# Optimization experiments

Hardware: AMD Instinct MI355X
Metric: run time of the kernel (lower is better)

## Reference

```python
import jax, jax.numpy as jnp
import numpy as np

B, N, I, O, R = 8, 1024, 256, 256, 8


def setup_inputs() -> dict:
    key = jax.random.key(0)
    k1, k2, k3 = jax.random.split(key, 3)
    x = jax.random.normal(k1, (B, N, I), dtype=jnp.float32)
    adj = jax.random.uniform(k2, (B, N, N, R), dtype=jnp.float32)  # soft adjacency [b, src, dst, r]
    weight = jax.random.normal(k3, (R, I, O), dtype=jnp.float32)   # per-relation transform
    return {"x": x, "adj": adj, "weight": weight}


def reference(x, adj, weight):
    # per-relation transformed features: [b, src, r, o]
    f = jnp.einsum('bni,rio->bnro', x, weight)
    # contraction over source nodes and relations, weighted by soft adjacency:
    # out[b, dst, o] = sum_{src, r} adj[b, src, dst, r] * f[b, src, r, o]
    out = jnp.einsum('bnro,bnmr->bmo', f, adj)
    # normalization: total incoming soft-edge weight per destination node
    denom = jnp.clip(adj.sum(axis=(1, 3)), 1e-16, None)  # [b, dst]
    return out / denom[..., None]
```

## Files before the change

### kernel.cpp

```cpp
#include <hip/hip_runtime.h>
#include <stdint.h>


typedef float          floatx4  __attribute__((ext_vector_type(4)));
typedef short          shortx8  __attribute__((ext_vector_type(8)));
typedef unsigned short ushortx4 __attribute__((ext_vector_type(4)));
typedef unsigned short ushortx8 __attribute__((ext_vector_type(8)));

__device__ __forceinline__ unsigned short f2bf(float f) {
  union { float f; unsigned int u; } v; v.f = f;
  unsigned int u = v.u + 0x7FFFu + ((v.u >> 16) & 1u);
  return (unsigned short)(u >> 16);
}

__device__ __forceinline__ void gload16(const void* g, void* l) {
  __builtin_amdgcn_global_load_lds((__attribute__((address_space(1))) void*)g,
                                   (__attribute__((address_space(3))) void*)l,
                                   16, 0, 0);
}

#define FENCE_KEEP4 asm volatile("s_waitcnt vmcnt(4) lgkmcnt(0)" ::: "memory")
#define FENCE_ALL   asm volatile("s_waitcnt vmcnt(0) lgkmcnt(0)" ::: "memory")
#define MEMFENCE    asm volatile("" ::: "memory")

__global__ __launch_bounds__(256) void prep_xw(const float* __restrict__ x,
                                               const float* __restrict__ w,
                                               unsigned short* __restrict__ xbf,
                                               unsigned short* __restrict__ wt) {
  int bid = blockIdx.x;
  if (bid < 1024) {
    int t = bid * 256 + threadIdx.x;
    const float4* p = (const float4*)x + (size_t)t * 2;
    float4 a = p[0], b4 = p[1];
    ushortx8 o;
    o[0] = f2bf(a.x);  o[1] = f2bf(a.y);  o[2] = f2bf(a.z);  o[3] = f2bf(a.w);
    o[4] = f2bf(b4.x); o[5] = f2bf(b4.y); o[6] = f2bf(b4.z); o[7] = f2bf(b4.w);
    *(ushortx8*)(xbf + (size_t)t * 8) = o;
  } else {
    int id = (bid - 1024) * 256 + threadIdx.x;
    int r = id >> 16, i = (id >> 8) & 255, o = id & 255;
    float v = w[((size_t)(r * 256 + i) << 8) + o];
    wt[((size_t)(o * 8 + r) << 8) + i] = f2bf(v);
  }
}

__global__ __launch_bounds__(256) void k1_gemm(const unsigned short* __restrict__ xbf,
                                               const unsigned short* __restrict__ wt,
                                               unsigned short* __restrict__ ft) {
  int bid = blockIdx.x;
  int p0 = (bid & 15) * 128, q0 = (bid >> 4) * 128;
  int l = threadIdx.x & 63, w = threadIdx.x >> 6;
  int lr = l & 15, lg = l >> 4;
  int pw = p0 + (w >> 1) * 64, qw = q0 + (w & 1) * 64;

  floatx4 acc[4][4] = {};
#pragma unroll
  for (int ks = 0; ks < 8; ++ks) {
    shortx8 a[4], b[4];
#pragma unroll
    for (int pi = 0; pi < 4; ++pi)
      a[pi] = *(const shortx8*)(wt + (size_t)(pw + pi * 16 + lr) * 256 + ks * 32 + lg * 8);
#pragma unroll
    for (int qi = 0; qi < 4; ++qi)
      b[qi] = *(const shortx8*)(xbf + (size_t)(qw + qi * 16 + lr) * 256 + ks * 32 + lg * 8);
#pragma unroll
    for (int pi = 0; pi < 4; ++pi)
#pragma unroll
      for (int qi = 0; qi < 4; ++qi)
        acc[pi][qi] = __builtin_amdgcn_mfma_f32_16x16x32_bf16(a[pi], b[qi], acc[pi][qi], 0, 0, 0);
  }
#pragma unroll
  for (int pi = 0; pi < 4; ++pi) {
    int nbase = pw + pi * 16 + lg * 4;
    int o = nbase >> 3, rb = nbase & 7;
#pragma unroll
    for (int qi = 0; qi < 4; ++qi) {
      int m = qw + qi * 16 + lr;
      int b8 = m >> 10, src = m & 1023;
      ushortx4 h;
      h[0] = f2bf(acc[pi][qi][0]); h[1] = f2bf(acc[pi][qi][1]);
      h[2] = f2bf(acc[pi][qi][2]); h[3] = f2bf(acc[pi][qi][3]);
      *(ushortx4*)(ft + ((size_t)(b8 * 256 + o) << 13) + src * 8 + rb) = h;
    }
  }
}

#define ASZ (64 * 64)
#define BSZ (128 * 64)
__global__ __launch_bounds__(512, 4) void k2_gemm(const float* __restrict__ adj,
                                                  const unsigned short* __restrict__ ft,
                                                  float* __restrict__ pout,
                                                  float* __restrict__ dpart) {
  __shared__ __align__(16) unsigned short Alds[3 * ASZ];
  __shared__ __align__(16) unsigned short Blds[3 * BSZ];

  int bid = blockIdx.x;
  int b = bid & 7;
  int o0 = ((bid >> 3) & 1) * 128;
  int kc = (bid >> 4) & 1;
  int dst0 = (bid >> 5) * 64;

  int t = threadIdx.x, l = t & 63, w = t >> 6;
  int lr = l & 15, lg = l >> 4;
  int wm = w >> 2, wo = w & 3;

  int dst_l = (t >> 1) & 63;
  int rh = (t & 1) * 4;
  int sA = t >> 7;
  int csw = (l & 7) ^ (l >> 3);

  const size_t adj_b = (size_t)b << 23;
  const unsigned short* ftb = ft + ((size_t)b << 21);
  const int src_base = kc * 512;

  float dsum = 0.f;
  floatx4 acc[2][2] = {};
  float4 av0[2], av1[2];

  auto A_load = [&](int kt, float4* v) {
#pragma unroll
    for (int j = 0; j < 2; ++j) {
      int src = src_base + kt * 8 + sA + j * 4;
      v[j] = *(const float4*)(adj + adj_b + ((size_t)src << 13)
                              + ((size_t)(dst0 + dst_l) << 3) + rh);
    }
  };
  auto A_store = [&](int buf, const float4* v) {
#pragma unroll
    for (int j = 0; j < 2; ++j) {
      int src_l = sA + j * 4;
      float4 q = v[j];
      dsum += q.x + q.y + q.z + q.w;
      ushortx4 h;
      h[0] = f2bf(q.x); h[1] = f2bf(q.y); h[2] = f2bf(q.z); h[3] = f2bf(q.w);
      int slot = src_l ^ (dst_l & 7);
      *(ushortx4*)&Alds[buf * ASZ + dst_l * 64 + slot * 8 + rh] = h;
    }
  };
  auto B_stage = [&](int kt, int buf) {
    int kbase = (src_base + kt * 8) * 8;
#pragma unroll
    for (int i = 0; i < 2; ++i) {
      int orow = w * 16 + i * 8 + (l >> 3);
      const unsigned short* g = ftb + ((size_t)(o0 + orow) << 13) + kbase + (csw << 3);
      gload16(g, &Blds[buf * BSZ + (w * 16 + i * 8) * 64]);
    }
  };
  auto compute = [&](int buf) {
#pragma unroll
    for (int s = 0; s < 2; ++s) {
      int slotbase = s * 4 + lg;
      shortx8 af[2], bfr[2];
#pragma unroll
      for (int mi = 0; mi < 2; ++mi) {
        int arow = wm * 32 + mi * 16 + lr;
        af[mi] = *(const shortx8*)&Alds[buf * ASZ + arow * 64 + ((slotbase ^ (arow & 7)) << 3)];
      }
#pragma unroll
      for (int ni = 0; ni < 2; ++ni) {
        int brow = wo * 32 + ni * 16 + lr;
        bfr[ni] = *(const shortx8*)&Blds[buf * BSZ + brow * 64 + ((slotbase ^ (brow & 7)) << 3)];
      }
#pragma unroll
      for (int mi = 0; mi < 2; ++mi)
#pragma unroll
        for (int ni = 0; ni < 2; ++ni)
          acc[mi][ni] = __builtin_amdgcn_mfma_f32_16x16x32_bf16(af[mi], bfr[ni], acc[mi][ni], 0, 0, 0);
    }
  };

#define STEP(kt, C0, C1, C2, RIN, ROUT, ISS, ST)                       \
  {                                                                    \
    if (ISS) { A_load((kt) + 2, ROUT); B_stage((kt) + 2, C2); }        \
    if (ST)  A_store(C1, RIN);                                         \
    compute(C0);                                                       \
    if (ST) {                                                          \
      if (ISS) { FENCE_KEEP4; } else { FENCE_ALL; }                    \
      __builtin_amdgcn_s_barrier();                                    \
      MEMFENCE;                                                        \
    }                                                                  \
  }

  B_stage(0, 0);
  A_load(0, av0);
  A_load(1, av1);
  B_stage(1, 1);
  A_store(0, av0);
  FENCE_KEEP4;
  __builtin_amdgcn_s_barrier();
  MEMFENCE;

  for (int kt0 = 0; kt0 < 60; kt0 += 6) {
    STEP(kt0 + 0, 0, 1, 2, av1, av0, 1, 1);
    STEP(kt0 + 1, 1, 2, 0, av0, av1, 1, 1);
    STEP(kt0 + 2, 2, 0, 1, av1, av0, 1, 1);
    STEP(kt0 + 3, 0, 1, 2, av0, av1, 1, 1);
    STEP(kt0 + 4, 1, 2, 0, av1, av0, 1, 1);
    STEP(kt0 + 5, 2, 0, 1, av0, av1, 1, 1);
  }
  STEP(60, 0, 1, 2, av1, av0, 1, 1);
  STEP(61, 1, 2, 0, av0, av1, 1, 1);
  STEP(62, 2, 0, 1, av1, av0, 0, 1);
  STEP(63, 0, 1, 2, av0, av1, 0, 0);
#undef STEP
  __syncthreads();

  float* dsf = (float*)Alds;
  dsf[t] = dsum;
  __syncthreads();
  if (t < 64) {
    float s = 0.f;
#pragma unroll
    for (int sl = 0; sl < 4; ++sl) {
      s += dsf[sl * 128 + t * 2];
      s += dsf[sl * 128 + t * 2 + 1];
    }
    dpart[kc * 8192 + (b << 10) + dst0 + t] = s;
  }

#pragma unroll
  for (int mi = 0; mi < 2; ++mi) {
#pragma unroll
    for (int reg = 0; reg < 4; ++reg) {
      int row = dst0 + wm * 32 + mi * 16 + lg * 4 + reg;
#pragma unroll
      for (int ni = 0; ni < 2; ++ni) {
        int col = o0 + wo * 32 + ni * 16 + lr;
        pout[(size_t)kc * 2097152 + (((size_t)b << 10) + row) * 256 + col] = acc[mi][ni][reg];
      }
    }
  }
}

__global__ __launch_bounds__(256) void k3_reduce(const float* __restrict__ pout,
                                                 const float* __restrict__ dpart,
                                                 float* __restrict__ outp) {
  int bid = blockIdx.x;
  size_t base = (size_t)bid * 256 + threadIdx.x;
  float v = pout[base] + pout[2097152 + base];
  float d = dpart[bid] + dpart[8192 + bid];
  outp[base] = v / fmaxf(d, 1e-16f);
}

extern "C" void kernel_launch(void* const* d_in, const int* in_sizes, int n_in,
                              void* d_out, int out_size, void* d_ws, size_t ws_size,
                              hipStream_t stream) {
  const float* x   = (const float*)d_in[0];
  const float* adj = (const float*)d_in[1];
  const float* w   = (const float*)d_in[2];
  float* out = (float*)d_out;

  char* ws = (char*)d_ws;
  unsigned short* ft  = (unsigned short*)(ws);
  unsigned short* xbf = (unsigned short*)(ws + 33554432);
  unsigned short* wt  = (unsigned short*)(ws + 37748736);
  float* pout  = (float*)(ws + 38797312);
  float* dpart = (float*)(ws + 55574528);

  prep_xw<<<3072, 256, 0, stream>>>(x, w, xbf, wt);
  k1_gemm<<<1024, 256, 0, stream>>>(xbf, wt, ft);
  k2_gemm<<<512, 512, 0, stream>>>(adj, ft, pout, dpart);
  k3_reduce<<<8192, 256, 0, stream>>>(pout, dpart, out);
}
```

Before: 137.0 us.

## Register-stage B tile and deepen prefetch to four A and three B tiles

Replaces the direct global-to-LDS loads of the B tile with ordinary global loads into registers, followed by swizzled LDS stores. The software pipeline is restructured around register prefetch queues four tiles deep for A and three for B, and LDS drops from triple to double buffering. Explicit vmcnt waits are removed so the compiler tracks outstanding loads. The bf16 packing now uses the HIP intrinsic two values at a time. The aim is more memory-latency hiding with less LDS, at the cost of more registers and extra LDS store instructions, which may reduce occupancy.

Result: slower. 202.4 us (+47.7%).

```diff
diff --git a/kernel.cpp b/kernel.cpp
--- a/kernel.cpp
+++ b/kernel.cpp
@@ -1,4 +1,5 @@
 #include <hip/hip_runtime.h>
+#include <hip/hip_bf16.h>
 #include <stdint.h>
 
 
@@ -6,6 +7,8 @@
 typedef short          shortx8  __attribute__((ext_vector_type(8)));
 typedef unsigned short ushortx4 __attribute__((ext_vector_type(4)));
 typedef unsigned short ushortx8 __attribute__((ext_vector_type(8)));
+typedef unsigned int   uintx2   __attribute__((ext_vector_type(2)));
+typedef unsigned int   uintx4   __attribute__((ext_vector_type(4)));
 
 __device__ __forceinline__ unsigned short f2bf(float f) {
   union { float f; unsigned int u; } v; v.f = f;
@@ -13,15 +16,14 @@
   return (unsigned short)(u >> 16);
 }
 
-__device__ __forceinline__ void gload16(const void* g, void* l) {
-  __builtin_amdgcn_global_load_lds((__attribute__((address_space(1))) void*)g,
-                                   (__attribute__((address_space(3))) void*)l,
-                                   16, 0, 0);
-}
-
-#define FENCE_KEEP4 asm volatile("s_waitcnt vmcnt(4) lgkmcnt(0)" ::: "memory")
-#define FENCE_ALL   asm volatile("s_waitcnt vmcnt(0) lgkmcnt(0)" ::: "memory")
-#define MEMFENCE    asm volatile("" ::: "memory")
+__device__ __forceinline__ unsigned int pkbf(float a, float b) {
+  __hip_bfloat16 ha = __float2bfloat16(a), hb = __float2bfloat16(b);
+  unsigned short ua, ub;
+  __builtin_memcpy(&ua, &ha, 2); __builtin_memcpy(&ub, &hb, 2);
+  return (unsigned int)ua | ((unsigned int)ub << 16);
+}
+
+#define MEMFENCE asm volatile("" ::: "memory")
 
 __global__ __launch_bounds__(256) void prep_xw(const float* __restrict__ x,
                                                const float* __restrict__ w,
@@ -91,8 +93,8 @@
                                                   const unsigned short* __restrict__ ft,
                                                   float* __restrict__ pout,
                                                   float* __restrict__ dpart) {
-  __shared__ __align__(16) unsigned short Alds[3 * ASZ];
-  __shared__ __align__(16) unsigned short Blds[3 * BSZ];
+  __shared__ __align__(16) unsigned short Alds[2 * ASZ];
+  __shared__ __align__(16) unsigned short Blds[2 * BSZ];
 
   int bid = blockIdx.x;
   int b = bid & 7;
@@ -107,15 +109,15 @@
   int dst_l = (t >> 1) & 63;
   int rh = (t & 1) * 4;
   int sA = t >> 7;
-  int csw = (l & 7) ^ (l >> 3);
 
   const size_t adj_b = (size_t)b << 23;
   const unsigned short* ftb = ft + ((size_t)b << 21);
   const int src_base = kc * 512;
 
-  float dsum = 0.f;
+  float d0 = 0.f, d1 = 0.f;
   floatx4 acc[2][2] = {};
-  float4 av0[2], av1[2];
+  float4 av0[2], av1[2], av2[2], av3[2];
+  uintx4 bv0[2], bv1[2], bv2[2];
 
   auto A_load = [&](int kt, float4* v) {
 #pragma unroll
@@ -130,20 +132,26 @@
     for (int j = 0; j < 2; ++j) {
       int src_l = sA + j * 4;
       float4 q = v[j];
-      dsum += q.x + q.y + q.z + q.w;
-      ushortx4 h;
-      h[0] = f2bf(q.x); h[1] = f2bf(q.y); h[2] = f2bf(q.z); h[3] = f2bf(q.w);
+      d0 += q.x + q.z; d1 += q.y + q.w;
+      uintx2 h; h[0] = pkbf(q.x, q.y); h[1] = pkbf(q.z, q.w);
       int slot = src_l ^ (dst_l & 7);
-      *(ushortx4*)&Alds[buf * ASZ + dst_l * 64 + slot * 8 + rh] = h;
-    }
-  };
-  auto B_stage = [&](int kt, int buf) {
+      *(uintx2*)&Alds[buf * ASZ + dst_l * 64 + slot * 8 + rh] = h;
+    }
+  };
+  auto B_load = [&](int kt, uintx4* v) {
     int kbase = (src_base + kt * 8) * 8;
 #pragma unroll
     for (int i = 0; i < 2; ++i) {
-      int orow = w * 16 + i * 8 + (l >> 3);
-      const unsigned short* g = ftb + ((size_t)(o0 + orow) << 13) + kbase + (csw << 3);
-      gload16(g, &Blds[buf * BSZ + (w * 16 + i * 8) * 64]);
+      int orow = o0 + w * 16 + i * 8 + (l >> 3);
+      v[i] = *(const uintx4*)(ftb + ((size_t)orow << 13) + kbase + ((l & 7) << 3));
+    }
+  };
+  auto B_store = [&](int buf, const uintx4* v) {
+#pragma unroll
+    for (int i = 0; i < 2; ++i) {
+      int row = w * 16 + i * 8 + (l >> 3);
+      int swc = (l & 7) ^ (l >> 3);
+      *(uintx4*)&Blds[buf * BSZ + row * 64 + swc * 8] = v[i];
     }
   };
   auto compute = [&](int buf) {
@@ -169,44 +177,49 @@
     }
   };
 
-#define STEP(kt, C0, C1, C2, RIN, ROUT, ISS, ST)                       \
+#define STEP(kt, AVL, AVS, BVL, BVS, CUR, NXT, ISSA, ISSB, ST)         \
   {                                                                    \
-    if (ISS) { A_load((kt) + 2, ROUT); B_stage((kt) + 2, C2); }        \
-    if (ST)  A_store(C1, RIN);                                         \
-    compute(C0);                                                       \
+    if (ISSA) A_load((kt) + 4, AVL);                                   \
+    if (ISSB) B_load((kt) + 3, BVL);                                   \
+    if (ST) { A_store(NXT, AVS); B_store(NXT, BVS); }                  \
+    compute(CUR);                                                      \
     if (ST) {                                                          \
-      if (ISS) { FENCE_KEEP4; } else { FENCE_ALL; }                    \
+      asm volatile("s_waitcnt lgkmcnt(0)" ::: "memory");               \
       __builtin_amdgcn_s_barrier();                                    \
       MEMFENCE;                                                        \
     }                                                                  \
   }
 
-  B_stage(0, 0);
-  A_load(0, av0);
-  A_load(1, av1);
-  B_stage(1, 1);
-  A_store(0, av0);
-  FENCE_KEEP4;
+  A_load(0, av0); A_load(1, av1); A_load(2, av2); A_load(3, av3);
+  B_load(0, bv0); B_load(1, bv1); B_load(2, bv2);
+  A_store(0, av0); B_store(0, bv0);
+  asm volatile("s_waitcnt lgkmcnt(0)" ::: "memory");
   __builtin_amdgcn_s_barrier();
   MEMFENCE;
 
-  for (int kt0 = 0; kt0 < 60; kt0 += 6) {
-    STEP(kt0 + 0, 0, 1, 2, av1, av0, 1, 1);
-    STEP(kt0 + 1, 1, 2, 0, av0, av1, 1, 1);
-    STEP(kt0 + 2, 2, 0, 1, av1, av0, 1, 1);
-    STEP(kt0 + 3, 0, 1, 2, av0, av1, 1, 1);
-    STEP(kt0 + 4, 1, 2, 0, av1, av0, 1, 1);
-    STEP(kt0 + 5, 2, 0, 1, av0, av1, 1, 1);
-  }
-  STEP(60, 0, 1, 2, av1, av0, 1, 1);
-  STEP(61, 1, 2, 0, av0, av1, 1, 1);
-  STEP(62, 2, 0, 1, av1, av0, 0, 1);
-  STEP(63, 0, 1, 2, av0, av1, 0, 0);
+  for (int kt0 = 0; kt0 < 60; kt0 += 12) {
+    STEP(kt0 + 0,  av0, av1, bv0, bv1, 0, 1, 1, 1, 1);
+    STEP(kt0 + 1,  av1, av2, bv1, bv2, 1, 0, 1, 1, 1);
+    STEP(kt0 + 2,  av2, av3, bv2, bv0, 0, 1, 1, 1, 1);
+    STEP(kt0 + 3,  av3, av0, bv0, bv1, 1, 0, 1, 1, 1);
+    STEP(kt0 + 4,  av0, av1, bv1, bv2, 0, 1, 1, 1, 1);
+    STEP(kt0 + 5,  av1, av2, bv2, bv0, 1, 0, 1, 1, 1);
+    STEP(kt0 + 6,  av2, av3, bv0, bv1, 0, 1, 1, 1, 1);
+    STEP(kt0 + 7,  av3, av0, bv1, bv2, 1, 0, 1, 1, 1);
+    STEP(kt0 + 8,  av0, av1, bv2, bv0, 0, 1, 1, 1, 1);
+    STEP(kt0 + 9,  av1, av2, bv0, bv1, 1, 0, 1, 1, 1);
+    STEP(kt0 + 10, av2, av3, bv1, bv2, 0, 1, 1, 1, 1);
+    STEP(kt0 + 11, av3, av0, bv2, bv0, 1, 0, 1, 1, 1);
+  }
+  STEP(60, av0, av1, bv0, bv1, 0, 1, 0, 1, 1);
+  STEP(61, av1, av2, bv1, bv2, 1, 0, 0, 0, 1);
+  STEP(62, av2, av3, bv2, bv0, 0, 1, 0, 0, 1);
+  STEP(63, av3, av0, bv0, bv1, 1, 0, 0, 0, 0);
 #undef STEP
   __syncthreads();
 
   float* dsf = (float*)Alds;
-  dsf[t] = dsum;
+  dsf[t] = d0 + d1;
   __syncthreads();
   if (t < 64) {
     float s = 0.f;
```

## Load adjacency directly into MFMA A-fragment registers, bypassing LDS staging

Applied to the files above, without the earlier changes.

Each wave now loads its own adjacency values from global memory straight into the register layout the MFMA A operand expects and converts them to bf16 in registers. This removes the A tile's LDS buffers, the LDS store and read traffic, and the final LDS reduction for the denominator, which is now done with wave shuffles. In exchange, the four waves sharing a row block each reload the same adjacency data instead of sharing it through LDS, raising global and cache traffic, and register pressure grows from holding two stages of float4 prefetches.

New measurement: 173.4 us. 1.27x slower.

```diff
diff --git a/kernel.cpp b/kernel.cpp
--- a/kernel.cpp
+++ b/kernel.cpp
@@ -1,4 +1,5 @@
 #include <hip/hip_runtime.h>
+#include <hip/hip_bf16.h>
 #include <stdint.h>
 
 
@@ -13,15 +14,22 @@
   return (unsigned short)(u >> 16);
 }
 
+__device__ __forceinline__ unsigned int pkbf(float a, float b) {
+  return ((unsigned int)f2bf(a)) | (((unsigned int)f2bf(b)) << 16);
+}
+
+__device__ __forceinline__ shortx8 cvt8(float4 a, float4 b) {
+  union { unsigned int u[4]; shortx8 s; } r;
+  r.u[0] = pkbf(a.x, a.y); r.u[1] = pkbf(a.z, a.w);
+  r.u[2] = pkbf(b.x, b.y); r.u[3] = pkbf(b.z, b.w);
+  return r.s;
+}
+
 __device__ __forceinline__ void gload16(const void* g, void* l) {
   __builtin_amdgcn_global_load_lds((__attribute__((address_space(1))) void*)g,
                                    (__attribute__((address_space(3))) void*)l,
                                    16, 0, 0);
 }
-
-#define FENCE_KEEP4 asm volatile("s_waitcnt vmcnt(4) lgkmcnt(0)" ::: "memory")
-#define FENCE_ALL   asm volatile("s_waitcnt vmcnt(0) lgkmcnt(0)" ::: "memory")
-#define MEMFENCE    asm volatile("" ::: "memory")
 
 __global__ __launch_bounds__(256) void prep_xw(const float* __restrict__ x,
                                                const float* __restrict__ w,
@@ -85,13 +93,11 @@
   }
 }
 
-#define ASZ (64 * 64)
 #define BSZ (128 * 64)
 __global__ __launch_bounds__(512, 4) void k2_gemm(const float* __restrict__ adj,
                                                   const unsigned short* __restrict__ ft,
                                                   float* __restrict__ pout,
                                                   float* __restrict__ dpart) {
-  __shared__ __align__(16) unsigned short Alds[3 * ASZ];
   __shared__ __align__(16) unsigned short Blds[3 * BSZ];
 
   int bid = blockIdx.x;
@@ -103,42 +109,30 @@
   int t = threadIdx.x, l = t & 63, w = t >> 6;
   int lr = l & 15, lg = l >> 4;
   int wm = w >> 2, wo = w & 3;
-
-  int dst_l = (t >> 1) & 63;
-  int rh = (t & 1) * 4;
-  int sA = t >> 7;
-  int csw = (l & 7) ^ (l >> 3);
-
-  const size_t adj_b = (size_t)b << 23;
+  bool wq0 = (wo == 0);
+
+  const int src_base = kc * 512;
+  const float* adjp = adj + ((size_t)b << 23) + ((size_t)src_base << 13)
+                    + ((size_t)(dst0 + wm * 32 + lr) << 3) + ((size_t)lg << 13);
   const unsigned short* ftb = ft + ((size_t)b << 21);
-  const int src_base = kc * 512;
-
-  float dsum = 0.f;
+
+  float dd[2] = {0.f, 0.f};
   floatx4 acc[2][2] = {};
-  float4 av0[2], av1[2];
-
-  auto A_load = [&](int kt, float4* v) {
-#pragma unroll
-    for (int j = 0; j < 2; ++j) {
-      int src = src_base + kt * 8 + sA + j * 4;
-      v[j] = *(const float4*)(adj + adj_b + ((size_t)src << 13)
-                              + ((size_t)(dst0 + dst_l) << 3) + rh);
-    }
-  };
-  auto A_store = [&](int buf, const float4* v) {
-#pragma unroll
-    for (int j = 0; j < 2; ++j) {
-      int src_l = sA + j * 4;
-      float4 q = v[j];
-      dsum += q.x + q.y + q.z + q.w;
-      ushortx4 h;
-      h[0] = f2bf(q.x); h[1] = f2bf(q.y); h[2] = f2bf(q.z); h[3] = f2bf(q.w);
-      int slot = src_l ^ (dst_l & 7);
-      *(ushortx4*)&Alds[buf * ASZ + dst_l * 64 + slot * 8 + rh] = h;
-    }
+  float4 aE[2][2][2], aO[2][2][2];
+
+  auto A_load = [&](int kt, float4 (&v)[2][2][2]) {
+#pragma unroll
+    for (int mi = 0; mi < 2; ++mi)
+#pragma unroll
+      for (int s = 0; s < 2; ++s)
+#pragma unroll
+        for (int j = 0; j < 2; ++j)
+          v[mi][s][j] = *(const float4*)(adjp + (size_t)kt * 65536
+                                         + s * 32768 + mi * 128 + j * 4);
   };
   auto B_stage = [&](int kt, int buf) {
     int kbase = (src_base + kt * 8) * 8;
+    int csw = (l & 7) ^ (l >> 3);
 #pragma unroll
     for (int i = 0; i < 2; ++i) {
       int orow = w * 16 + i * 8 + (l >> 3);
@@ -146,76 +140,71 @@
       gload16(g, &Blds[buf * BSZ + (w * 16 + i * 8) * 64]);
     }
   };
-  auto compute = [&](int buf) {
-#pragma unroll
-    for (int s = 0; s < 2; ++s) {
-      int slotbase = s * 4 + lg;
-      shortx8 af[2], bfr[2];
-#pragma unroll
-      for (int mi = 0; mi < 2; ++mi) {
-        int arow = wm * 32 + mi * 16 + lr;
-        af[mi] = *(const shortx8*)&Alds[buf * ASZ + arow * 64 + ((slotbase ^ (arow & 7)) << 3)];
-      }
-#pragma unroll
-      for (int ni = 0; ni < 2; ++ni) {
-        int brow = wo * 32 + ni * 16 + lr;
-        bfr[ni] = *(const shortx8*)&Blds[buf * BSZ + brow * 64 + ((slotbase ^ (brow & 7)) << 3)];
-      }
-#pragma unroll
-      for (int mi = 0; mi < 2; ++mi)
-#pragma unroll
-        for (int ni = 0; ni < 2; ++ni)
-          acc[mi][ni] = __builtin_amdgcn_mfma_f32_16x16x32_bf16(af[mi], bfr[ni], acc[mi][ni], 0, 0, 0);
-    }
-  };
-
-#define STEP(kt, C0, C1, C2, RIN, ROUT, ISS, ST)                       \
-  {                                                                    \
-    if (ISS) { A_load((kt) + 2, ROUT); B_stage((kt) + 2, C2); }        \
-    if (ST)  A_store(C1, RIN);                                         \
-    compute(C0);                                                       \
-    if (ST) {                                                          \
-      if (ISS) { FENCE_KEEP4; } else { FENCE_ALL; }                    \
-      __builtin_amdgcn_s_barrier();                                    \
-      MEMFENCE;                                                        \
-    }                                                                  \
+
+#define STEP(kt, C0, C1, C2, AC, ISS, ST)                                        \
+  {                                                                              \
+    if (ISS) B_stage((kt) + 2, C2);                                              \
+    __builtin_amdgcn_sched_barrier(0);                                           \
+    shortx8 af[2][2];                                                            \
+    _Pragma("unroll") for (int s = 0; s < 2; ++s)                                \
+      _Pragma("unroll") for (int mi = 0; mi < 2; ++mi) {                         \
+        float4 p = AC[mi][s][0], q = AC[mi][s][1];                               \
+        af[s][mi] = cvt8(p, q);                                                  \
+        if (wq0) dd[mi] += ((p.x + p.y) + (p.z + p.w)) + ((q.x + q.y) + (q.z + q.w)); \
+      }                                                                          \
+    if (ISS) A_load((kt) + 2, AC);                                               \
+    _Pragma("unroll") for (int s = 0; s < 2; ++s) {                              \
+      int slotbase = s * 4 + lg;                                                 \
+      shortx8 bfr[2];                                                            \
+      _Pragma("unroll") for (int ni = 0; ni < 2; ++ni) {                         \
+        int brow = wo * 32 + ni * 16 + lr;                                       \
+        bfr[ni] = *(const shortx8*)&Blds[(C0) * BSZ + brow * 64 + ((slotbase ^ (brow & 7)) << 3)]; \
+      }                                                                          \
+      _Pragma("unroll") for (int mi = 0; mi < 2; ++mi)                           \
+        _Pragma("unroll") for (int ni = 0; ni < 2; ++ni)                         \
+          acc[mi][ni] = __builtin_amdgcn_mfma_f32_16x16x32_bf16(af[s][mi], bfr[ni], acc[mi][ni], 0, 0, 0); \
+    }                                                                            \
+    if (ST) {                                                                    \
+      if (ISS) { asm volatile("s_waitcnt vmcnt(10)" ::: "memory"); }             \
+      else     { asm volatile("s_waitcnt vmcnt(0)"  ::: "memory"); }             \
+      __builtin_amdgcn_s_barrier();                                              \
+      asm volatile("" ::: "memory");                                             \
+    }                                                                            \
   }
 
   B_stage(0, 0);
-  A_load(0, av0);
-  A_load(1, av1);
   B_stage(1, 1);
-  A_store(0, av0);
-  FENCE_KEEP4;
+  __builtin_amdgcn_sched_barrier(0);
+  A_load(0, aE);
+  A_load(1, aO);
+  asm volatile("s_waitcnt vmcnt(0)" ::: "memory");
   __builtin_amdgcn_s_barrier();
-  MEMFENCE;
+  asm volatile("" ::: "memory");
 
   for (int kt0 = 0; kt0 < 60; kt0 += 6) {
-    STEP(kt0 + 0, 0, 1, 2, av1, av0, 1, 1);
-    STEP(kt0 + 1, 1, 2, 0, av0, av1, 1, 1);
-    STEP(kt0 + 2, 2, 0, 1, av1, av0, 1, 1);
-    STEP(kt0 + 3, 0, 1, 2, av0, av1, 1, 1);
-    STEP(kt0 + 4, 1, 2, 0, av1, av0, 1, 1);
-    STEP(kt0 + 5, 2, 0, 1, av0, av1, 1, 1);
-  }
-  STEP(60, 0, 1, 2, av1, av0, 1, 1);
-  STEP(61, 1, 2, 0, av0, av1, 1, 1);
-  STEP(62, 2, 0, 1, av1, av0, 0, 1);
-  STEP(63, 0, 1, 2, av0, av1, 0, 0);
+    STEP(kt0 + 0, 0, 1, 2, aE, 1, 1);
+    STEP(kt0 + 1, 1, 2, 0, aO, 1, 1);
+    STEP(kt0 + 2, 2, 0, 1, aE, 1, 1);
+    STEP(kt0 + 3, 0, 1, 2, aO, 1, 1);
+    STEP(kt0 + 4, 1, 2, 0, aE, 1, 1);
+    STEP(kt0 + 5, 2, 0, 1, aO, 1, 1);
+  }
+  STEP(60, 0, 1, 2, aE, 1, 1);
+  STEP(61, 1, 2, 0, aO, 1, 1);
+  STEP(62, 2, 0, 1, aE, 0, 1);
+  STEP(63, 0, 1, 2, aO, 0, 0);
 #undef STEP
-  __syncthreads();
-
-  float* dsf = (float*)Alds;
-  dsf[t] = dsum;
-  __syncthreads();
-  if (t < 64) {
-    float s = 0.f;
-#pragma unroll
-    for (int sl = 0; sl < 4; ++sl) {
-      s += dsf[sl * 128 + t * 2];
-      s += dsf[sl * 128 + t * 2 + 1];
-    }
-    dpart[kc * 8192 + (b << 10) + dst0 + t] = s;
+
+  if (wq0) {
+#pragma unroll
+    for (int mi = 0; mi < 2; ++mi) {
+      dd[mi] += __shfl_xor(dd[mi], 16);
+      dd[mi] += __shfl_xor(dd[mi], 32);
+    }
+    if (l < 16) {
+      dpart[kc * 8192 + (b << 10) + dst0 + wm * 32 + lr]      = dd[0];
+      dpart[kc * 8192 + (b << 10) + dst0 + wm * 32 + 16 + lr] = dd[1];
+    }
   }
 
 #pragma unroll
```

## Deepen k2 pipeline to prefetch distance three with 4-stage B buffers

Applied to the files above, without the earlier changes.

Restructures the k2 GEMM main loop so the B tile (bf16 transformed features) is staged three iterations ahead in four LDS buffers. The A tile (fp32 adjacency) moves to a double-buffered LDS layout whose loads are held in registers three steps ahead. Waits become vmcnt(8) with sched_barriers around the s_barrier, so more global loads stay in flight across each barrier. The bf16 conversion now uses the HIP intrinsic. This aims to hide global memory latency, at the cost of more LDS and registers per block, which could reduce occupancy.

New measurement: 134.1 us, median of 2. -2.1%, faster.

```diff
diff --git a/kernel.cpp b/kernel.cpp
--- a/kernel.cpp
+++ b/kernel.cpp
@@ -1,4 +1,5 @@
 #include <hip/hip_runtime.h>
+#include <hip/hip_bf16.h>
 #include <stdint.h>
 
 
@@ -8,9 +9,9 @@
 typedef unsigned short ushortx8 __attribute__((ext_vector_type(8)));
 
 __device__ __forceinline__ unsigned short f2bf(float f) {
-  union { float f; unsigned int u; } v; v.f = f;
-  unsigned int u = v.u + 0x7FFFu + ((v.u >> 16) & 1u);
-  return (unsigned short)(u >> 16);
+  __hip_bfloat16 h = __float2bfloat16(f);
+  unsigned short u; __builtin_memcpy(&u, &h, 2);
+  return u;
 }
 
 __device__ __forceinline__ void gload16(const void* g, void* l) {
@@ -18,10 +19,6 @@
                                    (__attribute__((address_space(3))) void*)l,
                                    16, 0, 0);
 }
-
-#define FENCE_KEEP4 asm volatile("s_waitcnt vmcnt(4) lgkmcnt(0)" ::: "memory")
-#define FENCE_ALL   asm volatile("s_waitcnt vmcnt(0) lgkmcnt(0)" ::: "memory")
-#define MEMFENCE    asm volatile("" ::: "memory")
 
 __global__ __launch_bounds__(256) void prep_xw(const float* __restrict__ x,
                                                const float* __restrict__ w,
@@ -85,14 +82,14 @@
   }
 }
 
-#define ASZ (64 * 64)
+#define ASZ 4096
 #define BSZ (128 * 64)
 __global__ __launch_bounds__(512, 4) void k2_gemm(const float* __restrict__ adj,
                                                   const unsigned short* __restrict__ ft,
                                                   float* __restrict__ pout,
                                                   float* __restrict__ dpart) {
-  __shared__ __align__(16) unsigned short Alds[3 * ASZ];
-  __shared__ __align__(16) unsigned short Blds[3 * BSZ];
+  __shared__ __align__(16) unsigned short Alds[2 * ASZ];
+  __shared__ __align__(16) unsigned short Blds[4 * BSZ];
 
   int bid = blockIdx.x;
   int b = bid & 7;
@@ -115,7 +112,7 @@
 
   float dsum = 0.f;
   floatx4 acc[2][2] = {};
-  float4 av0[2], av1[2];
+  float4 avA[2], avB[2];
 
   auto A_load = [&](int kt, float4* v) {
 #pragma unroll
@@ -125,7 +122,7 @@
                               + ((size_t)(dst0 + dst_l) << 3) + rh);
     }
   };
-  auto A_store = [&](int buf, const float4* v) {
+  auto A_store = [&](int abuf, const float4* v) {
 #pragma unroll
     for (int j = 0; j < 2; ++j) {
       int src_l = sA + j * 4;
@@ -134,7 +131,7 @@
       ushortx4 h;
       h[0] = f2bf(q.x); h[1] = f2bf(q.y); h[2] = f2bf(q.z); h[3] = f2bf(q.w);
       int slot = src_l ^ (dst_l & 7);
-      *(ushortx4*)&Alds[buf * ASZ + dst_l * 64 + slot * 8 + rh] = h;
+      *(ushortx4*)&Alds[abuf * ASZ + dst_l * 64 + slot * 8 + rh] = h;
     }
   };
   auto B_stage = [&](int kt, int buf) {
@@ -146,7 +143,7 @@
       gload16(g, &Blds[buf * BSZ + (w * 16 + i * 8) * 64]);
     }
   };
-  auto compute = [&](int buf) {
+  auto compute = [&](int bbuf, int abuf) {
 #pragma unroll
     for (int s = 0; s < 2; ++s) {
       int slotbase = s * 4 + lg;
@@ -154,12 +151,12 @@
 #pragma unroll
       for (int mi = 0; mi < 2; ++mi) {
         int arow = wm * 32 + mi * 16 + lr;
-        af[mi] = *(const shortx8*)&Alds[buf * ASZ + arow * 64 + ((slotbase ^ (arow & 7)) << 3)];
+        af[mi] = *(const shortx8*)&Alds[abuf * ASZ + arow * 64 + ((slotbase ^ (arow & 7)) << 3)];
       }
 #pragma unroll
       for (int ni = 0; ni < 2; ++ni) {
         int brow = wo * 32 + ni * 16 + lr;
-        bfr[ni] = *(const shortx8*)&Blds[buf * BSZ + brow * 64 + ((slotbase ^ (brow & 7)) << 3)];
+        bfr[ni] = *(const shortx8*)&Blds[bbuf * BSZ + brow * 64 + ((slotbase ^ (brow & 7)) << 3)];
       }
 #pragma unroll
       for (int mi = 0; mi < 2; ++mi)
@@ -169,39 +166,43 @@
     }
   };
 
-#define STEP(kt, C0, C1, C2, RIN, ROUT, ISS, ST)                       \
+#define STEP(kt, CUR, STG, ABN, ABC, AVx, ISS, STA, FN)                \
   {                                                                    \
-    if (ISS) { A_load((kt) + 2, ROUT); B_stage((kt) + 2, C2); }        \
-    if (ST)  A_store(C1, RIN);                                         \
-    compute(C0);                                                       \
-    if (ST) {                                                          \
-      if (ISS) { FENCE_KEEP4; } else { FENCE_ALL; }                    \
+    if (ISS) B_stage((kt) + 3, STG);                                   \
+    if (STA) A_store(ABN, AVx);                                        \
+    if (ISS) A_load((kt) + 3, AVx);                                    \
+    compute(CUR, ABC);                                                 \
+    if (FN >= 0) {                                                     \
+      __builtin_amdgcn_sched_barrier(0);                               \
+      if (FN == 8)      asm volatile("s_waitcnt vmcnt(8) lgkmcnt(0)" ::: "memory"); \
+      else if (FN == 4) asm volatile("s_waitcnt vmcnt(4) lgkmcnt(0)" ::: "memory"); \
+      else              asm volatile("s_waitcnt vmcnt(0) lgkmcnt(0)" ::: "memory"); \
       __builtin_amdgcn_s_barrier();                                    \
-      MEMFENCE;                                                        \
+      __builtin_amdgcn_sched_barrier(0);                               \
     }                                                                  \
   }
 
   B_stage(0, 0);
-  A_load(0, av0);
-  A_load(1, av1);
   B_stage(1, 1);
-  A_store(0, av0);
-  FENCE_KEEP4;
+  B_stage(2, 2);
+  A_load(0, avA);
+  A_store(0, avA);
+  A_load(1, avA);
+  A_load(2, avB);
+  asm volatile("s_waitcnt vmcnt(0) lgkmcnt(0)" ::: "memory");
   __builtin_amdgcn_s_barrier();
-  MEMFENCE;
-
-  for (int kt0 = 0; kt0 < 60; kt0 += 6) {
-    STEP(kt0 + 0, 0, 1, 2, av1, av0, 1, 1);
-    STEP(kt0 + 1, 1, 2, 0, av0, av1, 1, 1);
-    STEP(kt0 + 2, 2, 0, 1, av1, av0, 1, 1);
-    STEP(kt0 + 3, 0, 1, 2, av0, av1, 1, 1);
-    STEP(kt0 + 4, 1, 2, 0, av1, av0, 1, 1);
-    STEP(kt0 + 5, 2, 0, 1, av0, av1, 1, 1);
-  }
-  STEP(60, 0, 1, 2, av1, av0, 1, 1);
-  STEP(61, 1, 2, 0, av0, av1, 1, 1);
-  STEP(62, 2, 0, 1, av1, av0, 0, 1);
-  STEP(63, 0, 1, 2, av0, av1, 0, 0);
+  __builtin_amdgcn_sched_barrier(0);
+
+  for (int kt0 = 0; kt0 < 60; kt0 += 4) {
+    STEP(kt0 + 0, 0, 3, 1, 0, avA, 1, 1, 8);
+    STEP(kt0 + 1, 1, 0, 0, 1, avB, 1, 1, 8);
+    STEP(kt0 + 2, 2, 1, 1, 0, avA, 1, 1, 8);
+    STEP(kt0 + 3, 3, 2, 0, 1, avB, 1, 1, 8);
+  }
+  STEP(60, 0, 3, 1, 0, avA, 1, 1, 8);
+  STEP(61, 1, 0, 0, 1, avB, 0, 1, 4);
+  STEP(62, 2, 0, 1, 0, avA, 0, 1, 0);
+  STEP(63, 3, 0, 0, 1, avB, 0, 0, -1);
 #undef STEP
   __syncthreads();
 
```
